# Performance work log

Hardware: AMD Instinct MI355X
Metric: run time of the kernel (lower is better)

The kernel has to match this reference:

```python
import jax, jax.numpy as jnp
import numpy as np

N_NODES = 100000
N_EDGES = 1600000
D = 64


def _gcn_norm(edge_index, edge_weight, num_nodes):
    # PyG GCNConv default: add self-loops (weight 1), symmetric deg^-1/2 norm.
    src, dst = edge_index[0], edge_index[1]
    loop = jnp.arange(num_nodes, dtype=edge_index.dtype)
    src = jnp.concatenate([src, loop])
    dst = jnp.concatenate([dst, loop])
    w = jnp.concatenate([edge_weight, jnp.ones((num_nodes,), edge_weight.dtype)])
    deg = jax.ops.segment_sum(w, dst, num_segments=num_nodes)
    dinv = jnp.where(deg > 0, jax.lax.rsqrt(deg), 0.0)
    norm = dinv[src] * w * dinv[dst]  # [E + N]
    return src, dst, norm


def _gcn_conv(h, src, dst, norm, W, b, num_nodes):
    h = h @ W                                   # [N, C_out] linear transform first
    msg = h[src] * norm[:, None]                # gather + scale  [E+N, C_out]
    out = jax.ops.segment_sum(msg, dst, num_segments=num_nodes)  # scatter-add
    return out + b


def setup_inputs() -> dict:
    key = jax.random.key(0)
    ks = jax.random.split(key, 9)
    x = jax.random.normal(ks[0], (N_NODES, D), dtype=jnp.float32)
    edge_index = jax.random.randint(ks[1], (2, N_EDGES), 0, N_NODES, dtype=jnp.int32)
    edge_weight = jax.random.uniform(ks[2], (N_EDGES,), dtype=jnp.float32)
    s = 1.0 / np.sqrt(D)
    W1 = jax.random.uniform(ks[3], (D, D), jnp.float32, -s, s)
    b1 = jnp.zeros((D,), jnp.float32)
    W2 = jax.random.uniform(ks[4], (D, D), jnp.float32, -s, s)
    b2 = jnp.zeros((D,), jnp.float32)
    W3 = jax.random.uniform(ks[5], (D, 1), jnp.float32, -s, s)
    b3 = jnp.zeros((1,), jnp.float32)
    return {"x": x, "edge_index": edge_index, "edge_weight": edge_weight,
            "W1": W1, "b1": b1, "W2": W2, "b2": b2, "W3": W3, "b3": b3}


def reference(x, edge_index, edge_weight, W1, b1, W2, b2, W3, b3):
    n = x.shape[0]
    src, dst, norm = _gcn_norm(edge_index, edge_weight, n)
    h = _gcn_conv(x, src, dst, norm, W1, b1, n)
    h = jax.nn.relu(h)
    h = _gcn_conv(h, src, dst, norm, W2, b2, n)
    h = jax.nn.relu(h)
    h = _gcn_conv(h, src, dst, norm, W3, b3, n)
    return jax.nn.sigmoid(h)  # [N, 1]
```

## Files before the change

kernel.cpp:

```cpp
#include <hip/hip_runtime.h>
#include <hip/hip_fp16.h>
#include <math.h>

#define NN 100000
#define NE 1600000
#define D 64
#define BSH 8
#define NBIN 391
#define EB 8192
#define NBB ((NE + EB - 1) / EB)

typedef _Float16 f16x8 __attribute__((ext_vector_type(8)));
typedef float f32x4 __attribute__((ext_vector_type(4)));

__device__ __forceinline__ int2 ldnt2(const int2* p) {
    unsigned long long r = __builtin_nontemporal_load((const unsigned long long*)p);
    int2 o;
    o.x = (int)(unsigned)(r & 0xffffffffu);
    o.y = (int)(unsigned)(r >> 32);
    return o;
}

__global__ void k_binhist(const int* __restrict__ dst, int* __restrict__ counts, int E) {
    __shared__ int h[NBIN];
    for (int i = threadIdx.x; i < NBIN; i += blockDim.x) h[i] = 0;
    __syncthreads();
    int e0 = blockIdx.x * EB;
    int e1 = min(e0 + EB, E);
    for (int e = e0 + threadIdx.x; e < e1; e += blockDim.x)
        atomicAdd(&h[__builtin_nontemporal_load(dst + e) >> BSH], 1);
    __syncthreads();
    for (int i = threadIdx.x; i < NBIN; i += blockDim.x)
        counts[blockIdx.x * NBIN + i] = h[i];
}

__global__ void k_binscan(int* __restrict__ counts, int* __restrict__ binStart) {
    __shared__ int tot[512];
    int b = threadIdx.x;
    int sum = 0;
    if (b < NBIN) {
#pragma unroll 8
        for (int k = 0; k < NBB; k++) {
            int idx = k * NBIN + b;
            int c = counts[idx];
            counts[idx] = sum;
            sum += c;
        }
    }
    tot[b] = (b < NBIN) ? sum : 0;
    __syncthreads();
    int v = tot[b];
    for (int off = 1; off < 512; off <<= 1) {
        int add = (b >= off) ? tot[b - off] : 0;
        __syncthreads();
        tot[b] += add;
        __syncthreads();
    }
    if (b < NBIN) binStart[b] = tot[b] - v;
    if (b == NBIN - 1) binStart[NBIN] = tot[b];
}

__global__ void k_binscatter(const int* __restrict__ src, const int* __restrict__ dst,
                             const float* __restrict__ w, const int* __restrict__ counts,
                             const int* __restrict__ binStart, int2* __restrict__ binned,
                             int E) {
    __shared__ int cur[NBIN];
    for (int i = threadIdx.x; i < NBIN; i += blockDim.x)
        cur[i] = binStart[i] + counts[blockIdx.x * NBIN + i];
    __syncthreads();
    int e0 = blockIdx.x * EB;
    int e1 = min(e0 + EB, E);
    for (int e = e0 + threadIdx.x; e < e1; e += blockDim.x) {
        int d = __builtin_nontemporal_load(dst + e);
        int s = __builtin_nontemporal_load(src + e);
        float wv = __builtin_nontemporal_load(w + e);
        int pos = atomicAdd(&cur[d >> BSH], 1);
        binned[pos] = make_int2(((d & 255) << 17) | s, __float_as_int(wv));
    }
}

__global__ void k_degcsr(const int2* __restrict__ binned, const int* __restrict__ binStart,
                         float* __restrict__ dinv, int* __restrict__ row_ptr,
                         int2* __restrict__ edges, int n) {
    __shared__ int   cnt[256];
    __shared__ float ws[256];
    __shared__ int   off[256];
    __shared__ int   rp[256];
    __shared__ float dd[256];
    int b = blockIdx.x, t = threadIdx.x;
    cnt[t] = 0; ws[t] = 0.0f;
    __syncthreads();
    int e0 = binStart[b], e1 = binStart[b + 1];
    for (int e = e0 + t; e < e1; e += 256) {
        int2 r = binned[e];
        int dlow = (unsigned)r.x >> 17;
        atomicAdd(&cnt[dlow], 1);
        atomicAdd(&ws[dlow], __int_as_float(r.y));
    }
    __syncthreads();
    int v = cnt[t];
    off[t] = v;
    __syncthreads();
    for (int o = 1; o < 256; o <<= 1) {
        int add = (t >= o) ? off[t - o] : 0;
        __syncthreads();
        off[t] += add;
        __syncthreads();
    }
    int node = b * 256 + t;
    float dvv = rsqrtf(1.0f + ws[t]);
    rp[t] = e0 + off[t] - v;
    dd[t] = dvv;
    if (node < n) { dinv[node] = dvv; row_ptr[node] = rp[t]; }
    if (b == NBIN - 1 && t == 0) row_ptr[n] = binStart[NBIN];
    cnt[t] = 0;
    __syncthreads();
    for (int e = e0 + t; e < e1; e += 256) {
        int2 r = binned[e];
        int dlow = (unsigned)r.x >> 17;
        int s = r.x & 0x1FFFF;
        int rank = atomicAdd(&cnt[dlow], 1);
        float nv = __int_as_float(r.y) * dd[dlow];
        edges[rp[dlow] + rank] = make_int2(s, __float_as_int(nv));
    }
}

template <int IN_HALF>
__global__ void k_gemm(const void* __restrict__ Xv, const float* __restrict__ W,
                       const float* __restrict__ dinv, __half* __restrict__ T, int n) {
    int wid = (int)((blockIdx.x * blockDim.x + threadIdx.x) >> 6);
    int lane = threadIdx.x & 63;
    int col16 = lane & 15, kg = lane >> 4;
    int r0 = wid * 32;
    if (r0 >= n) return;
    f16x8 bf[2][4];
#pragma unroll
    for (int kk = 0; kk < 2; kk++)
#pragma unroll
        for (int ct = 0; ct < 4; ct++) {
            f16x8 b;
#pragma unroll
            for (int j = 0; j < 8; j++)
                b[j] = (_Float16)W[(size_t)(kk * 32 + kg * 8 + j) * D + ct * 16 + col16];
            bf[kk][ct] = b;
        }
#pragma unroll
    for (int tt = 0; tt < 2; tt++) {
        int row = r0 + tt * 16 + col16;
        f16x8 a0, a1;
        if (IN_HALF) {
            const _Float16* xr = (const _Float16*)Xv + (size_t)row * D;
            a0 = *(const f16x8*)(xr + kg * 8);
            a1 = *(const f16x8*)(xr + 32 + kg * 8);
        } else {
            const float* xr = (const float*)Xv + (size_t)row * D;
#pragma unroll
            for (int j = 0; j < 8; j++) {
                a0[j] = (_Float16)xr[kg * 8 + j];
                a1[j] = (_Float16)xr[32 + kg * 8 + j];
            }
        }
        float dvr[4];
#pragma unroll
        for (int r = 0; r < 4; r++) dvr[r] = dinv[r0 + tt * 16 + kg * 4 + r];
#pragma unroll
        for (int ct = 0; ct < 4; ct++) {
            f32x4 z = {0.0f, 0.0f, 0.0f, 0.0f};
            z = __builtin_amdgcn_mfma_f32_16x16x32_f16(a0, bf[0][ct], z, 0, 0, 0);
            z = __builtin_amdgcn_mfma_f32_16x16x32_f16(a1, bf[1][ct], z, 0, 0, 0);
            __half* to = T + (size_t)(r0 + tt * 16 + kg * 4) * D + ct * 16 + col16;
#pragma unroll
            for (int r = 0; r < 4; r++)
                to[(size_t)r * D] = __float2half(z[r] * dvr[r]);
        }
    }
}

template <int FUSE_W3>
__global__ void k_agg(const __half2* __restrict__ T2, const int* __restrict__ row_ptr,
                      const int2* __restrict__ edges, const float* __restrict__ dinv,
                      const float* __restrict__ bias, const float* __restrict__ W3,
                      void* __restrict__ outv, int n) {
    int wave = (int)((blockIdx.x * blockDim.x + threadIdx.x) >> 6);
    int lane = threadIdx.x & 63;
    if (wave >= n) return;
    int c = lane & 31;
    int h = lane >> 5;
    int beg = row_ptr[wave], end = row_ptr[wave + 1];
    float ax = 0.0f, ay = 0.0f, bx = 0.0f, by = 0.0f;
    int i = beg;
    for (; i + 16 <= end; i += 16) {
        int2 er[8];
#pragma unroll
        for (int j = 0; j < 8; j++) er[j] = ldnt2(&edges[i + 2 * j + h]);
        __half2 tv[8];
#pragma unroll
        for (int j = 0; j < 8; j++) tv[j] = T2[(size_t)er[j].x * 32 + c];
#pragma unroll
        for (int j = 0; j < 8; j++) {
            float nv = __int_as_float(er[j].y);
            float2 f = __half22float2(tv[j]);
            if (j & 1) { bx += nv * f.x; by += nv * f.y; }
            else       { ax += nv * f.x; ay += nv * f.y; }
        }
    }
    if (i + 8 <= end) {
        int2 er[4];
#pragma unroll
        for (int j = 0; j < 4; j++) er[j] = ldnt2(&edges[i + 2 * j + h]);
        __half2 tv[4];
#pragma unroll
        for (int j = 0; j < 4; j++) tv[j] = T2[(size_t)er[j].x * 32 + c];
#pragma unroll
        for (int j = 0; j < 4; j++) {
            float nv = __int_as_float(er[j].y);
            float2 f = __half22float2(tv[j]);
            if (j & 1) { bx += nv * f.x; by += nv * f.y; }
            else       { ax += nv * f.x; ay += nv * f.y; }
        }
        i += 8;
    }
    if (i + 4 <= end) {
        int2 er[2];
#pragma unroll
        for (int j = 0; j < 2; j++) er[j] = ldnt2(&edges[i + 2 * j + h]);
#pragma unroll
        for (int j = 0; j < 2; j++) {
            float nv = __int_as_float(er[j].y);
            float2 f = __half22float2(T2[(size_t)er[j].x * 32 + c]);
            if (j & 1) { bx += nv * f.x; by += nv * f.y; }
            else       { ax += nv * f.x; ay += nv * f.y; }
        }
        i += 4;
    }
    if (i + 2 <= end) {
        int2 e = ldnt2(&edges[i + h]);
        float nv = __int_as_float(e.y);
        float2 f = __half22float2(T2[(size_t)e.x * 32 + c]);
        ax += nv * f.x; ay += nv * f.y;
        i += 2;
    }
    if (i < end && h == 0) {
        int2 e = ldnt2(&edges[i]);
        float nv = __int_as_float(e.y);
        float2 f = __half22float2(T2[(size_t)e.x * 32 + c]);
        ax += nv * f.x; ay += nv * f.y;
    }
    ax += bx; ay += by;
    ax += __shfl_xor(ax, 32);
    ay += __shfl_xor(ay, 32);
    float dv = dinv[wave];
    float2 self = __half22float2(T2[(size_t)wave * 32 + c]);
    float hx = fmaxf(ax + dv * self.x + bias[2 * c], 0.0f);
    float hy = fmaxf(ay + dv * self.y + bias[2 * c + 1], 0.0f);
    if (FUSE_W3) {
        float pp = hx * W3[2 * c] + hy * W3[2 * c + 1];
#pragma unroll
        for (int off = 16; off; off >>= 1) pp += __shfl_xor(pp, off);
        if (lane == 0) ((float*)outv)[wave] = dv * pp;
    } else {
        if (lane < 32) ((__half2*)outv)[(size_t)wave * 32 + c] = __floats2half2_rn(hx, hy);
    }
}

__global__ void k_agg3(const float* __restrict__ t3, const int* __restrict__ row_ptr,
                       const int2* __restrict__ edges, const float* __restrict__ dinv,
                       const float* __restrict__ b3, float* __restrict__ out, int n) {
    int v = blockIdx.x * blockDim.x + threadIdx.x;
    if (v >= n) return;
    float dv = dinv[v];
    float acc0 = dv * t3[v];
    float acc1 = 0.0f;
    int beg = row_ptr[v], end = row_ptr[v + 1];
    int i = beg;
    for (; i + 8 <= end; i += 8) {
        int2 er[8]; float av[8];
#pragma unroll
        for (int j = 0; j < 8; j++) er[j] = ldnt2(&edges[i + j]);
#pragma unroll
        for (int j = 0; j < 8; j++) av[j] = t3[er[j].x];
#pragma unroll
        for (int j = 0; j < 8; j++) {
            if (j & 1) acc1 += __int_as_float(er[j].y) * av[j];
            else       acc0 += __int_as_float(er[j].y) * av[j];
        }
    }
    for (; i < end; i++) {
        int2 e = ldnt2(&edges[i]);
        acc0 += __int_as_float(e.y) * t3[e.x];
    }
    float z = acc0 + acc1 + b3[0];
    out[v] = 1.0f / (1.0f + expf(-z));
}

extern "C" void kernel_launch(void* const* d_in, const int* in_sizes, int n_in,
                              void* d_out, int out_size, void* d_ws, size_t ws_size,
                              hipStream_t stream) {
    const float* x  = (const float*)d_in[0];
    const int*   ei = (const int*)d_in[1];
    const float* w  = (const float*)d_in[2];
    const float* W1 = (const float*)d_in[3];
    const float* b1 = (const float*)d_in[4];
    const float* W2 = (const float*)d_in[5];
    const float* b2 = (const float*)d_in[6];
    const float* W3 = (const float*)d_in[7];
    const float* b3 = (const float*)d_in[8];
    float* out = (float*)d_out;

    const int N = NN, E = NE;
    const int* src = ei;
    const int* dst = ei + E;

    char* p = (char*)d_ws;
    auto alloc = [&](size_t bytes) -> char* {
        char* r = p;
        p += (bytes + 255) & ~(size_t)255;
        return r;
    };
    float* dinv    = (float*)alloc((size_t)N * 4);
    int*   row_ptr = (int*)alloc((size_t)(N + 1) * 4);
    int*   binStart= (int*)alloc((NBIN + 1) * 4);
    int*   counts  = (int*)alloc((size_t)NBB * NBIN * 4);
    int2*  binned  = (int2*)alloc((size_t)E * 8);
    int2*  edges   = (int2*)alloc((size_t)E * 8);
    __half* bufA   = (__half*)alloc((size_t)N * D * 2);
    __half* bufB   = (__half*)alloc((size_t)N * D * 2);
    float* t3      = (float*)alloc((size_t)N * 4);

    const int BT = 256;
    int gN = (N + BT - 1) / BT;
    int gW = (N * 64 + BT - 1) / BT;
    int nWaves = (N + 31) / 32;
    int gG = (nWaves * 64 + BT - 1) / BT;

    k_binhist<<<NBB, BT, 0, stream>>>(dst, counts, E);
    k_binscan<<<1, 512, 0, stream>>>(counts, binStart);
    k_binscatter<<<NBB, BT, 0, stream>>>(src, dst, w, counts, binStart, binned, E);
    k_degcsr<<<NBIN, BT, 0, stream>>>(binned, binStart, dinv, row_ptr, edges, N);

    k_gemm<0><<<gG, BT, 0, stream>>>(x, W1, dinv, bufA, N);
    k_agg<0><<<gW, BT, 0, stream>>>((const __half2*)bufA, row_ptr, edges, dinv, b1, nullptr, bufB, N);
    k_gemm<1><<<gG, BT, 0, stream>>>(bufB, W2, dinv, bufA, N);
    k_agg<1><<<gW, BT, 0, stream>>>((const __half2*)bufA, row_ptr, edges, dinv, b2, W3, t3, N);
    k_agg3<<<gN, BT, 0, stream>>>(t3, row_ptr, edges, dinv, b3, out, N);
}
```

Before: 223.7 us.

## Store edge norms as packed half2 and accumulate aggregation in fp16 FMA

Edge norm values are now stored as a duplicated half2 in the CSR edge array. The aggregation kernel accumulates with packed __hfma2 instead of converting to fp32 and doing scalar FMAs, which roughly halves the ALU instructions in the gather loop. Separately, the binning histogram and scatter kernels use 128-bit vector loads that handle four edges per thread. The risks are fp16 accumulation error over long edge lists, and an assumption that each block's edge range is 4-aligned, which holds for EB=8192 and NE=1.6M.

```diff
diff --git a/kernel.cpp b/kernel.cpp
--- a/kernel.cpp
+++ b/kernel.cpp
@@ -12,6 +12,8 @@
 
 typedef _Float16 f16x8 __attribute__((ext_vector_type(8)));
 typedef float f32x4 __attribute__((ext_vector_type(4)));
+typedef int   i32x4 __attribute__((ext_vector_type(4)));
+typedef float fl32x4 __attribute__((ext_vector_type(4)));
 
 __device__ __forceinline__ int2 ldnt2(const int2* p) {
     unsigned long long r = __builtin_nontemporal_load((const unsigned long long*)p);
@@ -21,14 +23,22 @@
     return o;
 }
 
+__device__ __forceinline__ int h2i(__half2 v) { return *(int*)&v; }
+__device__ __forceinline__ __half2 i2h(int v) { return *(__half2*)&v; }
+
 __global__ void k_binhist(const int* __restrict__ dst, int* __restrict__ counts, int E) {
     __shared__ int h[NBIN];
     for (int i = threadIdx.x; i < NBIN; i += blockDim.x) h[i] = 0;
     __syncthreads();
     int e0 = blockIdx.x * EB;
     int e1 = min(e0 + EB, E);
-    for (int e = e0 + threadIdx.x; e < e1; e += blockDim.x)
-        atomicAdd(&h[__builtin_nontemporal_load(dst + e) >> BSH], 1);
+    for (int e = e0 + (int)threadIdx.x * 4; e < e1; e += blockDim.x * 4) {
+        i32x4 d4 = __builtin_nontemporal_load((const i32x4*)(dst + e));
+        atomicAdd(&h[d4.x >> BSH], 1);
+        atomicAdd(&h[d4.y >> BSH], 1);
+        atomicAdd(&h[d4.z >> BSH], 1);
+        atomicAdd(&h[d4.w >> BSH], 1);
+    }
     __syncthreads();
     for (int i = threadIdx.x; i < NBIN; i += blockDim.x)
         counts[blockIdx.x * NBIN + i] = h[i];
@@ -70,12 +80,19 @@
     __syncthreads();
     int e0 = blockIdx.x * EB;
     int e1 = min(e0 + EB, E);
-    for (int e = e0 + threadIdx.x; e < e1; e += blockDim.x) {
-        int d = __builtin_nontemporal_load(dst + e);
-        int s = __builtin_nontemporal_load(src + e);
-        float wv = __builtin_nontemporal_load(w + e);
-        int pos = atomicAdd(&cur[d >> BSH], 1);
-        binned[pos] = make_int2(((d & 255) << 17) | s, __float_as_int(wv));
+    for (int e = e0 + (int)threadIdx.x * 4; e < e1; e += blockDim.x * 4) {
+        i32x4  d4 = __builtin_nontemporal_load((const i32x4*)(dst + e));
+        i32x4  s4 = __builtin_nontemporal_load((const i32x4*)(src + e));
+        fl32x4 w4 = __builtin_nontemporal_load((const fl32x4*)(w + e));
+        int pos;
+        pos = atomicAdd(&cur[d4.x >> BSH], 1);
+        binned[pos] = make_int2(((d4.x & 255) << 17) | s4.x, __float_as_int(w4.x));
+        pos = atomicAdd(&cur[d4.y >> BSH], 1);
+        binned[pos] = make_int2(((d4.y & 255) << 17) | s4.y, __float_as_int(w4.y));
+        pos = atomicAdd(&cur[d4.z >> BSH], 1);
+        binned[pos] = make_int2(((d4.z & 255) << 17) | s4.z, __float_as_int(w4.z));
+        pos = atomicAdd(&cur[d4.w >> BSH], 1);
+        binned[pos] = make_int2(((d4.w & 255) << 17) | s4.w, __float_as_int(w4.w));
     }
 }
 
@@ -121,7 +138,8 @@
         int s = r.x & 0x1FFFF;
         int rank = atomicAdd(&cnt[dlow], 1);
         float nv = __int_as_float(r.y) * dd[dlow];
-        edges[rp[dlow] + rank] = make_int2(s, __float_as_int(nv));
+        __half2 nh = __floats2half2_rn(nv, nv);
+        edges[rp[dlow] + rank] = make_int2(s, h2i(nh));
     }
 }
 
@@ -187,7 +205,8 @@
     int c = lane & 31;
     int h = lane >> 5;
     int beg = row_ptr[wave], end = row_ptr[wave + 1];
-    float ax = 0.0f, ay = 0.0f, bx = 0.0f, by = 0.0f;
+    __half2 accA = __floats2half2_rn(0.0f, 0.0f);
+    __half2 accB = accA;
     int i = beg;
     for (; i + 16 <= end; i += 16) {
         int2 er[8];
@@ -198,10 +217,9 @@
         for (int j = 0; j < 8; j++) tv[j] = T2[(size_t)er[j].x * 32 + c];
 #pragma unroll
         for (int j = 0; j < 8; j++) {
-            float nv = __int_as_float(er[j].y);
-            float2 f = __half22float2(tv[j]);
-            if (j & 1) { bx += nv * f.x; by += nv * f.y; }
-            else       { ax += nv * f.x; ay += nv * f.y; }
+            __half2 ev2 = i2h(er[j].y);
+            if (j & 1) accB = __hfma2(ev2, tv[j], accB);
+            else       accA = __hfma2(ev2, tv[j], accA);
         }
     }
     if (i + 8 <= end) {
@@ -213,10 +231,9 @@
         for (int j = 0; j < 4; j++) tv[j] = T2[(size_t)er[j].x * 32 + c];
 #pragma unroll
         for (int j = 0; j < 4; j++) {
-            float nv = __int_as_float(er[j].y);
-            float2 f = __half22float2(tv[j]);
-            if (j & 1) { bx += nv * f.x; by += nv * f.y; }
-            else       { ax += nv * f.x; ay += nv * f.y; }
+            __half2 ev2 = i2h(er[j].y);
+            if (j & 1) accB = __hfma2(ev2, tv[j], accB);
+            else       accA = __hfma2(ev2, tv[j], accA);
         }
         i += 8;
     }
@@ -226,27 +243,25 @@
         for (int j = 0; j < 2; j++) er[j] = ldnt2(&edges[i + 2 * j + h]);
 #pragma unroll
         for (int j = 0; j < 2; j++) {
-            float nv = __int_as_float(er[j].y);
-            float2 f = __half22float2(T2[(size_t)er[j].x * 32 + c]);
-            if (j & 1) { bx += nv * f.x; by += nv * f.y; }
-            else       { ax += nv * f.x; ay += nv * f.y; }
+            __half2 ev2 = i2h(er[j].y);
+            __half2 tvj = T2[(size_t)er[j].x * 32 + c];
+            if (j & 1) accB = __hfma2(ev2, tvj, accB);
+            else       accA = __hfma2(ev2, tvj, accA);
         }
         i += 4;
     }
     if (i + 2 <= end) {
         int2 e = ldnt2(&edges[i + h]);
-        float nv = __int_as_float(e.y);
-        float2 f = __half22float2(T2[(size_t)e.x * 32 + c]);
-        ax += nv * f.x; ay += nv * f.y;
+        accA = __hfma2(i2h(e.y), T2[(size_t)e.x * 32 + c], accA);
         i += 2;
     }
     if (i < end && h == 0) {
         int2 e = ldnt2(&edges[i]);
-        float nv = __int_as_float(e.y);
-        float2 f = __half22float2(T2[(size_t)e.x * 32 + c]);
-        ax += nv * f.x; ay += nv * f.y;
-    }
-    ax += bx; ay += by;
+        accB = __hfma2(i2h(e.y), T2[(size_t)e.x * 32 + c], accB);
+    }
+    float2 fa = __half22float2(accA);
+    float2 fb = __half22float2(accB);
+    float ax = fa.x + fb.x, ay = fa.y + fb.y;
     ax += __shfl_xor(ax, 32);
     ay += __shfl_xor(ay, 32);
     float dv = dinv[wave];
@@ -281,13 +296,14 @@
         for (int j = 0; j < 8; j++) av[j] = t3[er[j].x];
 #pragma unroll
         for (int j = 0; j < 8; j++) {
-            if (j & 1) acc1 += __int_as_float(er[j].y) * av[j];
-            else       acc0 += __int_as_float(er[j].y) * av[j];
+            float ev = __low2float(i2h(er[j].y));
+            if (j & 1) acc1 += ev * av[j];
+            else       acc0 += ev * av[j];
         }
     }
     for (; i < end; i++) {
         int2 e = ldnt2(&edges[i]);
-        acc0 += __int_as_float(e.y) * t3[e.x];
+        acc0 += __low2float(i2h(e.y)) * t3[e.x];
     }
     float z = acc0 + acc1 + b3[0];
     out[v] = 1.0f / (1.0f + expf(-z));
```

Result: slower. 241.4 us (+7.9%).

## Merge CSR build kernels into one cooperative kernel with grid syncs

Applied to the files above, without the earlier changes.

Combines the bin histogram, bin scan, bin scatter and degree/CSR kernels into one cooperative launch of NBB blocks, with grid.sync between phases, so three launch boundaries disappear. The edge loads are also widened to 4-element vector nontemporal loads, and the bin scan now uses wave shuffles instead of a block-wide shared-memory scan. The CSR phase now runs on only NBB (196) blocks looping over 391 bins, which gives less parallelism than the old 391-block launch. The single-block scan phase leaves the rest of the grid idle at the barrier.

```diff
diff --git a/kernel.cpp b/kernel.cpp
--- a/kernel.cpp
+++ b/kernel.cpp
@@ -1,6 +1,9 @@
 #include <hip/hip_runtime.h>
 #include <hip/hip_fp16.h>
+#include <hip/hip_cooperative_groups.h>
 #include <math.h>
+
+namespace cg = cooperative_groups;
 
 #define NN 100000
 #define NE 1600000
@@ -12,6 +15,8 @@
 
 typedef _Float16 f16x8 __attribute__((ext_vector_type(8)));
 typedef float f32x4 __attribute__((ext_vector_type(4)));
+typedef int   i32x4 __attribute__((ext_vector_type(4)));
+typedef float fl32x4 __attribute__((ext_vector_type(4)));
 
 __device__ __forceinline__ int2 ldnt2(const int2* p) {
     unsigned long long r = __builtin_nontemporal_load((const unsigned long long*)p);
@@ -21,107 +26,124 @@
     return o;
 }
 
-__global__ void k_binhist(const int* __restrict__ dst, int* __restrict__ counts, int E) {
-    __shared__ int h[NBIN];
-    for (int i = threadIdx.x; i < NBIN; i += blockDim.x) h[i] = 0;
+__global__ void k_csrbuild(const int* __restrict__ src, const int* __restrict__ dst,
+                           const float* __restrict__ w, int* __restrict__ counts,
+                           int* __restrict__ binStart, int2* __restrict__ binned,
+                           float* __restrict__ dinv, int* __restrict__ row_ptr,
+                           int2* __restrict__ edges, int E, int n) {
+    cg::grid_group grid = cg::this_grid();
+    __shared__ int lds[1280];
+    int bid = blockIdx.x, t = threadIdx.x;
+    int e0 = bid * EB;
+    int e1 = min(e0 + EB, E);
+
+    for (int i = t; i < NBIN; i += 256) lds[i] = 0;
     __syncthreads();
-    int e0 = blockIdx.x * EB;
-    int e1 = min(e0 + EB, E);
-    for (int e = e0 + threadIdx.x; e < e1; e += blockDim.x)
-        atomicAdd(&h[__builtin_nontemporal_load(dst + e) >> BSH], 1);
+    for (int e = e0 + t * 4; e < e1; e += 256 * 4) {
+        i32x4 d4 = __builtin_nontemporal_load((const i32x4*)(dst + e));
+        atomicAdd(&lds[d4.x >> BSH], 1);
+        atomicAdd(&lds[d4.y >> BSH], 1);
+        atomicAdd(&lds[d4.z >> BSH], 1);
+        atomicAdd(&lds[d4.w >> BSH], 1);
+    }
     __syncthreads();
-    for (int i = threadIdx.x; i < NBIN; i += blockDim.x)
-        counts[blockIdx.x * NBIN + i] = h[i];
-}
-
-__global__ void k_binscan(int* __restrict__ counts, int* __restrict__ binStart) {
-    __shared__ int tot[512];
-    int b = threadIdx.x;
-    int sum = 0;
-    if (b < NBIN) {
-#pragma unroll 8
-        for (int k = 0; k < NBB; k++) {
-            int idx = k * NBIN + b;
-            int c = counts[idx];
-            counts[idx] = sum;
-            sum += c;
-        }
-    }
-    tot[b] = (b < NBIN) ? sum : 0;
+    for (int i = t; i < NBIN; i += 256) counts[bid * NBIN + i] = lds[i];
+    grid.sync();
+
+    if (bid == 0) {
+        lds[t] = 0; lds[t + 256] = 0;
+        __syncthreads();
+        for (int b = t; b < NBIN; b += 256) {
+            int sum = 0;
+            for (int k = 0; k < NBB; k++) {
+                int idx = k * NBIN + b;
+                int c = counts[idx];
+                counts[idx] = sum;
+                sum += c;
+            }
+            lds[b] = sum;
+        }
+        __syncthreads();
+        if (t < 64) {
+            int lane = t, carry = 0;
+            for (int base = 0; base < NBIN; base += 64) {
+                int idx = base + lane;
+                int orig = (idx < NBIN) ? lds[idx] : 0;
+                int v = orig;
+#pragma unroll
+                for (int o = 1; o < 64; o <<= 1) {
+                    int u = __shfl_up(v, o);
+                    if (lane >= o) v += u;
+                }
+                if (idx < NBIN) binStart[idx] = carry + v - orig;
+                carry += __shfl(v, 63);
+            }
+            if (lane == 0) binStart[NBIN] = carry;
+        }
+    }
+    grid.sync();
+
+    for (int i = t; i < NBIN; i += 256)
+        lds[i] = binStart[i] + counts[bid * NBIN + i];
     __syncthreads();
-    int v = tot[b];
-    for (int off = 1; off < 512; off <<= 1) {
-        int add = (b >= off) ? tot[b - off] : 0;
-        __syncthreads();
-        tot[b] += add;
-        __syncthreads();
-    }
-    if (b < NBIN) binStart[b] = tot[b] - v;
-    if (b == NBIN - 1) binStart[NBIN] = tot[b];
-}
-
-__global__ void k_binscatter(const int* __restrict__ src, const int* __restrict__ dst,
-                             const float* __restrict__ w, const int* __restrict__ counts,
-                             const int* __restrict__ binStart, int2* __restrict__ binned,
-                             int E) {
-    __shared__ int cur[NBIN];
-    for (int i = threadIdx.x; i < NBIN; i += blockDim.x)
-        cur[i] = binStart[i] + counts[blockIdx.x * NBIN + i];
-    __syncthreads();
-    int e0 = blockIdx.x * EB;
-    int e1 = min(e0 + EB, E);
-    for (int e = e0 + threadIdx.x; e < e1; e += blockDim.x) {
-        int d = __builtin_nontemporal_load(dst + e);
-        int s = __builtin_nontemporal_load(src + e);
-        float wv = __builtin_nontemporal_load(w + e);
-        int pos = atomicAdd(&cur[d >> BSH], 1);
-        binned[pos] = make_int2(((d & 255) << 17) | s, __float_as_int(wv));
-    }
-}
-
-__global__ void k_degcsr(const int2* __restrict__ binned, const int* __restrict__ binStart,
-                         float* __restrict__ dinv, int* __restrict__ row_ptr,
-                         int2* __restrict__ edges, int n) {
-    __shared__ int   cnt[256];
-    __shared__ float ws[256];
-    __shared__ int   off[256];
-    __shared__ int   rp[256];
-    __shared__ float dd[256];
-    int b = blockIdx.x, t = threadIdx.x;
-    cnt[t] = 0; ws[t] = 0.0f;
-    __syncthreads();
-    int e0 = binStart[b], e1 = binStart[b + 1];
-    for (int e = e0 + t; e < e1; e += 256) {
-        int2 r = binned[e];
-        int dlow = (unsigned)r.x >> 17;
-        atomicAdd(&cnt[dlow], 1);
-        atomicAdd(&ws[dlow], __int_as_float(r.y));
-    }
-    __syncthreads();
-    int v = cnt[t];
-    off[t] = v;
-    __syncthreads();
-    for (int o = 1; o < 256; o <<= 1) {
-        int add = (t >= o) ? off[t - o] : 0;
-        __syncthreads();
-        off[t] += add;
-        __syncthreads();
-    }
-    int node = b * 256 + t;
-    float dvv = rsqrtf(1.0f + ws[t]);
-    rp[t] = e0 + off[t] - v;
-    dd[t] = dvv;
-    if (node < n) { dinv[node] = dvv; row_ptr[node] = rp[t]; }
-    if (b == NBIN - 1 && t == 0) row_ptr[n] = binStart[NBIN];
-    cnt[t] = 0;
-    __syncthreads();
-    for (int e = e0 + t; e < e1; e += 256) {
-        int2 r = binned[e];
-        int dlow = (unsigned)r.x >> 17;
-        int s = r.x & 0x1FFFF;
-        int rank = atomicAdd(&cnt[dlow], 1);
-        float nv = __int_as_float(r.y) * dd[dlow];
-        edges[rp[dlow] + rank] = make_int2(s, __float_as_int(nv));
+    for (int e = e0 + t * 4; e < e1; e += 256 * 4) {
+        i32x4  d4 = __builtin_nontemporal_load((const i32x4*)(dst + e));
+        i32x4  s4 = __builtin_nontemporal_load((const i32x4*)(src + e));
+        fl32x4 w4 = __builtin_nontemporal_load((const fl32x4*)(w + e));
+        int pos;
+        pos = atomicAdd(&lds[d4.x >> BSH], 1);
+        binned[pos] = make_int2(((d4.x & 255) << 17) | s4.x, __float_as_int(w4.x));
+        pos = atomicAdd(&lds[d4.y >> BSH], 1);
+        binned[pos] = make_int2(((d4.y & 255) << 17) | s4.y, __float_as_int(w4.y));
+        pos = atomicAdd(&lds[d4.z >> BSH], 1);
+        binned[pos] = make_int2(((d4.z & 255) << 17) | s4.z, __float_as_int(w4.z));
+        pos = atomicAdd(&lds[d4.w >> BSH], 1);
+        binned[pos] = make_int2(((d4.w & 255) << 17) | s4.w, __float_as_int(w4.w));
+    }
+    grid.sync();
+
+    int*   cnt = lds;
+    float* ws  = (float*)(lds + 256);
+    int*   off = lds + 512;
+    int*   rp  = lds + 768;
+    float* dd  = (float*)(lds + 1024);
+    for (int b = bid; b < NBIN; b += NBB) {
+        __syncthreads();
+        cnt[t] = 0; ws[t] = 0.0f;
+        __syncthreads();
+        int be0 = binStart[b], be1 = binStart[b + 1];
+        for (int e = be0 + t; e < be1; e += 256) {
+            int2 r = binned[e];
+            int dlow = (unsigned)r.x >> 17;
+            atomicAdd(&cnt[dlow], 1);
+            atomicAdd(&ws[dlow], __int_as_float(r.y));
+        }
+        __syncthreads();
+        int v = cnt[t];
+        off[t] = v;
+        __syncthreads();
+        for (int o = 1; o < 256; o <<= 1) {
+            int add = (t >= o) ? off[t - o] : 0;
+            __syncthreads();
+            off[t] += add;
+            __syncthreads();
+        }
+        int node = b * 256 + t;
+        float dvv = rsqrtf(1.0f + ws[t]);
+        rp[t] = be0 + off[t] - v;
+        dd[t] = dvv;
+        if (node < n) { dinv[node] = dvv; row_ptr[node] = rp[t]; }
+        if (b == NBIN - 1 && t == 0) row_ptr[n] = binStart[NBIN];
+        cnt[t] = 0;
+        __syncthreads();
+        for (int e = be0 + t; e < be1; e += 256) {
+            int2 r = binned[e];
+            int dlow = (unsigned)r.x >> 17;
+            int s = r.x & 0x1FFFF;
+            int rank = atomicAdd(&cnt[dlow], 1);
+            float nv = __int_as_float(r.y) * dd[dlow];
+            edges[rp[dlow] + rank] = make_int2(s, __float_as_int(nv));
+        }
     }
 }
 
@@ -307,7 +329,7 @@
     const float* b3 = (const float*)d_in[8];
     float* out = (float*)d_out;
 
-    const int N = NN, E = NE;
+    int N = NN, E = NE;
     const int* src = ei;
     const int* dst = ei + E;
 
@@ -333,10 +355,10 @@
     int nWaves = (N + 31) / 32;
     int gG = (nWaves * 64 + BT - 1) / BT;
 
-    k_binhist<<<NBB, BT, 0, stream>>>(dst, counts, E);
-    k_binscan<<<1, 512, 0, stream>>>(counts, binStart);
-    k_binscatter<<<NBB, BT, 0, stream>>>(src, dst, w, counts, binStart, binned, E);
-    k_degcsr<<<NBIN, BT, 0, stream>>>(binned, binStart, dinv, row_ptr, edges, N);
+    void* args[] = {(void*)&src, (void*)&dst, (void*)&w, (void*)&counts, (void*)&binStart,
+                    (void*)&binned, (void*)&dinv, (void*)&row_ptr, (void*)&edges,
+                    (void*)&E, (void*)&N};
+    hipLaunchCooperativeKernel((void*)k_csrbuild, dim3(NBB), dim3(BT), args, 0, stream);
 
     k_gemm<0><<<gG, BT, 0, stream>>>(x, W1, dinv, bufA, N);
     k_agg<0><<<gW, BT, 0, stream>>>((const __half2*)bufA, row_ptr, edges, dinv, b1, nullptr, bufB, N);
```

After: 294.1 us. +31.4%, slower.
